# Kernel optimization log

Measured on AMD Instinct MI355X. Metric: run time of the kernel, lower is better.

The kernel has to match this reference:

```python
import jax, jax.numpy as jnp
import numpy as np

D1, D2, HIDDEN, BATCH = 8, 8, 256, 131072
SCALE_LIMIT = 1.0


def _mlp(h, w1, b1, w2, b2, w3, b3):
    # Linear-ReLU-Linear-ReLU-Linear, torch Linear convention: y = h @ W.T + b
    h = jax.nn.relu(h @ w1.T + b1)
    h = jax.nn.relu(h @ w2.T + b2)
    return h @ w3.T + b3


def setup_inputs() -> dict:
    key = jax.random.key(0)
    ks = jax.random.split(key, 25)
    inp = {"x": jax.random.normal(ks[0], (BATCH, D1 + D2), dtype=jnp.float32)}
    i = 1
    for net, d_in, d_out in (("s1", D2, D1), ("t1", D2, D1), ("s2", D1, D2), ("t2", D1, D2)):
        for lname, (o, nin) in (("1", (HIDDEN, d_in)), ("2", (HIDDEN, HIDDEN)), ("3", (d_out, HIDDEN))):
            lim = 1.0 / np.sqrt(nin)  # torch default init range
            inp[f"{net}_w{lname}"] = jax.random.uniform(ks[i], (o, nin), jnp.float32, -lim, lim); i += 1
            inp[f"{net}_b{lname}"] = jnp.zeros((o,), jnp.float32)
    return inp


def reference(x,
              s1_w1, s1_b1, s1_w2, s1_b2, s1_w3, s1_b3,
              t1_w1, t1_b1, t1_w2, t1_b2, t1_w3, t1_b3,
              s2_w1, s2_b1, s2_w2, s2_b2, s2_w3, s2_b3,
              t2_w1, t2_b1, t2_w2, t2_b2, t2_w3, t2_b3):
    x1, x2 = x[:, :D1], x[:, D1:]
    # first half-coupling: transform x1 conditioned on x2
    s2 = jnp.tanh(_mlp(x2, s1_w1, s1_b1, s1_w2, s1_b2, s1_w3, s1_b3)) * SCALE_LIMIT
    t2 = _mlp(x2, t1_w1, t1_b1, t1_w2, t1_b2, t1_w3, t1_b3)
    y1 = x1 * jnp.exp(s2) + t2
    # second half-coupling: transform x2 conditioned on y1
    s1 = jnp.tanh(_mlp(y1, s2_w1, s2_b1, s2_w2, s2_b2, s2_w3, s2_b3)) * SCALE_LIMIT
    t1 = _mlp(y1, t2_w1, t2_b1, t2_w2, t2_b2, t2_w3, t2_b3)
    y2 = x2 * jnp.exp(s1) + t1
    y = jnp.concatenate([y1, y2], axis=1)
    log_det = s2.sum(axis=1) + s1.sum(axis=1)
    return y, log_det
```

## Files before the change

### kernel.cpp

```cpp
#include <hip/hip_runtime.h>

#define BATCHN 131072
#define M_TILE 128
#define NTHREADS 1024
#define HPITCH 280
#define W2P_OFF 4096
#define W3P_OFF 73728
#define NET_STRIDE 77824
#define PACK_TOTAL (4 * NET_STRIDE)

typedef _Float16 hv8 __attribute__((ext_vector_type(8)));
typedef _Float16 hv4 __attribute__((ext_vector_type(4)));
typedef __fp16  fp16x2 __attribute__((ext_vector_type(2)));
typedef float f32x16 __attribute__((ext_vector_type(16)));
typedef float f32x4  __attribute__((ext_vector_type(4)));

struct __align__(16) SMEM {
    _Float16 xin[M_TILE][16];
    _Float16 Ha[M_TILE][HPITCH];
    _Float16 Hb[M_TILE][HPITCH];
    float s_tile[M_TILE][8];
    float t_tile[M_TILE][8];
    float ldet[M_TILE];
};

__global__ __launch_bounds__(256) void pack_weights(
    const float* __restrict__ s1w1, const float* __restrict__ s1b1, const float* __restrict__ s1w2, const float* __restrict__ s1b2, const float* __restrict__ s1w3,
    const float* __restrict__ t1w1, const float* __restrict__ t1b1, const float* __restrict__ t1w2, const float* __restrict__ t1b2, const float* __restrict__ t1w3,
    const float* __restrict__ s2w1, const float* __restrict__ s2b1, const float* __restrict__ s2w2, const float* __restrict__ s2b2, const float* __restrict__ s2w3,
    const float* __restrict__ t2w1, const float* __restrict__ t2b1, const float* __restrict__ t2w2, const float* __restrict__ t2b2, const float* __restrict__ t2w3,
    _Float16* __restrict__ wp)
{
    int tid = blockIdx.x * 256 + threadIdx.x;
    if (tid >= PACK_TOTAL) return;
    int net = tid / NET_STRIDE;
    int rem = tid - net * NET_STRIDE;
    const float* w1 = (net == 0) ? s1w1 : (net == 1) ? t1w1 : (net == 2) ? s2w1 : t2w1;
    const float* b1 = (net == 0) ? s1b1 : (net == 1) ? t1b1 : (net == 2) ? s2b1 : t2b1;
    const float* w2 = (net == 0) ? s1w2 : (net == 1) ? t1w2 : (net == 2) ? s2w2 : t2w2;
    const float* b2 = (net == 0) ? s1b2 : (net == 1) ? t1b2 : (net == 2) ? s2b2 : t2b2;
    const float* w3 = (net == 0) ? s1w3 : (net == 1) ? t1w3 : (net == 2) ? s2w3 : t2w3;
    float val;
    if (rem < W2P_OFF) {
        int nt = rem >> 9;
        int l  = (rem >> 3) & 63, j = rem & 7;
        int n  = nt * 32 + (l & 31);
        int k  = ((l >> 5) << 3) + j;
        val = (k < 8) ? w1[n * 8 + k] : (k == 8 ? b1[n] : 0.0f);
    } else if (rem < W3P_OFF) {
        int r = rem - W2P_OFF;
        int chunk = r >> 9;
        int nt = chunk / 17, ks = chunk - nt * 17;
        int l = (r >> 3) & 63, j = r & 7;
        int n = nt * 32 + (l & 31);
        int kk = ((l >> 5) << 3) + j;
        val = (ks < 16) ? w2[n * 256 + ks * 16 + kk] : (kk == 0 ? b2[n] : 0.0f);
    } else {
        int r = rem - W3P_OFF;
        int ks = r >> 9;
        int l = (r >> 3) & 63, j = r & 7;
        int n = l & 15;
        int k = ks * 32 + ((l >> 4) & 3) * 8 + j;
        val = (n < 8) ? w3[n * 256 + k] : 0.0f;
    }
    wp[tid] = (_Float16)val;
}

#define MFMA32(A,B,C) __builtin_amdgcn_mfma_f32_32x32x16_f16((A),(B),(C),0,0,0)

__device__ __forceinline__ void epi4(_Float16* __restrict__ dst, const f32x16& acc)
{
    #pragma unroll
    for (int q = 0; q < 4; ++q) {
        union { hv4 h4; fp16x2 h2[2]; } u;
        u.h2[0] = __builtin_amdgcn_cvt_pkrtz(fmaxf(acc[4*q+0], 0.f), fmaxf(acc[4*q+1], 0.f));
        u.h2[1] = __builtin_amdgcn_cvt_pkrtz(fmaxf(acc[4*q+2], 0.f), fmaxf(acc[4*q+3], 0.f));
        *(hv4*)(dst + 8 * q) = u.h4;
    }
}

__device__ __forceinline__ void layer1(const _Float16* __restrict__ wp, SMEM& sm,
                                       int nt, int mt, int lane, int l31, int hi)
{
    hv8 a  = *(const hv8*)(wp + nt * 512 + lane * 8);
    hv8 b0 = *(const hv8*)(&sm.xin[mt * 64 + l31][hi * 8]);
    hv8 b1 = *(const hv8*)(&sm.xin[mt * 64 + 32 + l31][hi * 8]);
    f32x16 z = {};
    f32x16 acc0 = MFMA32(a, b0, z);
    f32x16 acc1 = MFMA32(a, b1, z);
    epi4(&sm.Ha[mt * 64 + l31][nt * 32 + 4 * hi], acc0);
    epi4(&sm.Ha[mt * 64 + 32 + l31][nt * 32 + 4 * hi], acc1);
}

__device__ __forceinline__ void layer2(const _Float16* __restrict__ wp, SMEM& sm,
                                       int nt, int mt, int lane, int l31, int hi)
{
    const _Float16* __restrict__ w2 = wp + W2P_OFF + nt * (17 * 512);
    hv8 w[17];
    #pragma unroll
    for (int ks = 0; ks < 17; ++ks) w[ks] = *(const hv8*)(w2 + ks * 512 + lane * 8);
    const _Float16* __restrict__ bb0 = &sm.Ha[mt * 64 + l31][hi * 8];
    const _Float16* __restrict__ bb1 = &sm.Ha[mt * 64 + 32 + l31][hi * 8];
    f32x16 acc0 = {}, acc1 = {};
    #pragma unroll
    for (int ks = 0; ks < 17; ++ks) {
        hv8 b0 = *(const hv8*)(bb0 + ks * 16);
        hv8 b1 = *(const hv8*)(bb1 + ks * 16);
        acc0 = MFMA32(w[ks], b0, acc0);
        acc1 = MFMA32(w[ks], b1, acc1);
    }
    epi4(&sm.Hb[mt * 64 + l31][nt * 32 + 4 * hi], acc0);
    epi4(&sm.Hb[mt * 64 + 32 + l31][nt * 32 + 4 * hi], acc1);
}

template <bool IS_S>
__device__ __forceinline__ void layer3(const _Float16* __restrict__ wp, const float* __restrict__ b3,
                                       SMEM& sm, float (*__restrict__ stile)[8],
                                       int wave, int lane)
{
    if (wave >= 8) return;
    const _Float16* __restrict__ w3 = wp + W3P_OFF;
    const int l15 = lane & 15, q = lane >> 4;
    const int m = wave * 16 + l15;
    hv8 w[8];
    #pragma unroll
    for (int ks = 0; ks < 8; ++ks) w[ks] = *(const hv8*)(w3 + ks * 512 + lane * 8);
    const _Float16* __restrict__ bb = &sm.Hb[m][q * 8];
    f32x4 acc = {};
    #pragma unroll
    for (int ks = 0; ks < 8; ++ks)
        acc = __builtin_amdgcn_mfma_f32_16x16x32_f16(w[ks], *(const hv8*)(bb + ks * 32), acc, 0, 0, 0);
    if (q < 2) {
        float4 bv = *(const float4*)(b3 + q * 4);
        float o0 = acc[0] + bv.x, o1 = acc[1] + bv.y, o2 = acc[2] + bv.z, o3 = acc[3] + bv.w;
        if (IS_S) { o0 = tanhf(o0); o1 = tanhf(o1); o2 = tanhf(o2); o3 = tanhf(o3); }
        *(float4*)&stile[m][q * 4] = make_float4(o0, o1, o2, o3);
    }
}

__device__ __forceinline__ void stage(const _Float16* __restrict__ wpS, const float* __restrict__ b3S,
                                      const _Float16* __restrict__ wpT, const float* __restrict__ b3T,
                                      SMEM& sm,
                                      int wave, int nt, int mt, int lane, int l31, int hi)
{
    layer1(wpS, sm, nt, mt, lane, l31, hi);
    __syncthreads();
    layer2(wpS, sm, nt, mt, lane, l31, hi);
    __syncthreads();
    layer1(wpT, sm, nt, mt, lane, l31, hi);
    layer3<true >(wpS, b3S, sm, sm.s_tile, wave, lane);
    __syncthreads();
    layer2(wpT, sm, nt, mt, lane, l31, hi);
    __syncthreads();
    layer3<false>(wpT, b3T, sm, sm.t_tile, wave, lane);
    __syncthreads();
}

__global__ __launch_bounds__(NTHREADS, 4) void coupling_kernel(
    const float* __restrict__ x, const _Float16* __restrict__ wp,
    const float* __restrict__ s1b3, const float* __restrict__ t1b3,
    const float* __restrict__ s2b3, const float* __restrict__ t2b3,
    float* __restrict__ out)
{
    __shared__ SMEM sm;
    const int tid  = threadIdx.x;
    const int wave = tid >> 6, lane = tid & 63;
    const int l31  = lane & 31, hi = lane >> 5;
    const int mt   = wave & 1, nt = wave >> 1;
    const long row0 = (long)blockIdx.x * M_TILE;

    #pragma unroll
    for (int e = tid; e < M_TILE * 16; e += NTHREADS) {
        int row = e >> 4, c = e & 15;
        float v = (c < 8) ? x[(row0 + row) * 16 + 8 + c] : (c == 8 ? 1.0f : 0.0f);
        sm.xin[row][c] = (_Float16)v;
        sm.Ha[row][256 + c] = (c == 0) ? (_Float16)1.0f : (_Float16)0.0f;
    }
    __syncthreads();

    stage(wp + 0 * NET_STRIDE, s1b3, wp + 1 * NET_STRIDE, t1b3, sm, wave, nt, mt, lane, l31, hi);

    {
        int row = tid >> 3, c = tid & 7;
        float s = sm.s_tile[row][c];
        float t = sm.t_tile[row][c];
        float x1 = x[(row0 + row) * 16 + c];
        float y = x1 * expf(s) + t;
        out[(row0 + row) * 16 + c] = y;
        sm.xin[row][c] = (_Float16)y;
    }
    if (tid < M_TILE) {
        float a = 0.f;
        #pragma unroll
        for (int c = 0; c < 8; ++c) a += sm.s_tile[tid][c];
        sm.ldet[tid] = a;
    }
    __syncthreads();

    stage(wp + 2 * NET_STRIDE, s2b3, wp + 3 * NET_STRIDE, t2b3, sm, wave, nt, mt, lane, l31, hi);

    {
        int row = tid >> 3, c = tid & 7;
        float s = sm.s_tile[row][c];
        float t = sm.t_tile[row][c];
        float x2 = x[(row0 + row) * 16 + 8 + c];
        out[(row0 + row) * 16 + 8 + c] = x2 * expf(s) + t;
    }
    if (tid < M_TILE) {
        float a = sm.ldet[tid];
        #pragma unroll
        for (int c = 0; c < 8; ++c) a += sm.s_tile[tid][c];
        out[(long)BATCHN * 16 + row0 + tid] = a;
    }
}

extern "C" void kernel_launch(void* const* d_in, const int* in_sizes, int n_in,
                              void* d_out, int out_size, void* d_ws, size_t ws_size,
                              hipStream_t stream)
{
    const float* x = (const float*)d_in[0];
    const float* s1w1 = (const float*)d_in[1];  const float* s1b1 = (const float*)d_in[2];
    const float* s1w2 = (const float*)d_in[3];  const float* s1b2 = (const float*)d_in[4];
    const float* s1w3 = (const float*)d_in[5];  const float* s1b3 = (const float*)d_in[6];
    const float* t1w1 = (const float*)d_in[7];  const float* t1b1 = (const float*)d_in[8];
    const float* t1w2 = (const float*)d_in[9];  const float* t1b2 = (const float*)d_in[10];
    const float* t1w3 = (const float*)d_in[11]; const float* t1b3 = (const float*)d_in[12];
    const float* s2w1 = (const float*)d_in[13]; const float* s2b1 = (const float*)d_in[14];
    const float* s2w2 = (const float*)d_in[15]; const float* s2b2 = (const float*)d_in[16];
    const float* s2w3 = (const float*)d_in[17]; const float* s2b3 = (const float*)d_in[18];
    const float* t2w1 = (const float*)d_in[19]; const float* t2b1 = (const float*)d_in[20];
    const float* t2w2 = (const float*)d_in[21]; const float* t2b2 = (const float*)d_in[22];
    const float* t2w3 = (const float*)d_in[23]; const float* t2b3 = (const float*)d_in[24];

    _Float16* wp = (_Float16*)d_ws;

    pack_weights<<<(PACK_TOTAL + 255) / 256, 256, 0, stream>>>(
        s1w1, s1b1, s1w2, s1b2, s1w3,
        t1w1, t1b1, t1w2, t1b2, t1w3,
        s2w1, s2b1, s2w2, s2b2, s2w3,
        t2w1, t2b1, t2w2, t2b2, t2w3, wp);

    coupling_kernel<<<BATCHN / M_TILE, NTHREADS, 0, stream>>>(
        x, wp, s1b3, t1b3, s2b3, t2b3, (float*)d_out);
}
```

Baseline: 196.1 us.

## Halve block to 512 threads with 2x2 MFMA register tiles per wave

Block size drops from 1024 to 512 threads, so each wave now computes a 64x64 output tile (two N-tiles by two M-tiles) instead of 64x32. The goal is to reuse each LDS B-operand load across two weight fragments, and the W2 pack layout is reordered to interleave pairs of N-tiles. W2 weights (34 fragments) are preloaded into registers before layer1 so the global loads overlap with layer1 and the barrier. This raises register pressure, with launch bounds lowered to 2 blocks per CU and 34 hv8 live registers, which may reduce occupancy.

```diff
diff --git a/kernel.cpp b/kernel.cpp
--- a/kernel.cpp
+++ b/kernel.cpp
@@ -2,7 +2,7 @@
 
 #define BATCHN 131072
 #define M_TILE 128
-#define NTHREADS 1024
+#define NTHREADS 512
 #define HPITCH 280
 #define W2P_OFF 4096
 #define W3P_OFF 73728
@@ -50,7 +50,9 @@
     } else if (rem < W3P_OFF) {
         int r = rem - W2P_OFF;
         int chunk = r >> 9;
-        int nt = chunk / 17, ks = chunk - nt * 17;
+        int g = chunk / 34, rr = chunk - g * 34;
+        int ks = rr >> 1, s = rr & 1;
+        int nt = 2 * g + s;
         int l = (r >> 3) & 63, j = r & 7;
         int n = nt * 32 + (l & 31);
         int kk = ((l >> 5) << 3) + j;
@@ -79,38 +81,59 @@
     }
 }
 
+__device__ __forceinline__ void preloadW2(const _Float16* __restrict__ w2pp, int lane, hv8 (&w)[34])
+{
+    #pragma unroll
+    for (int i = 0; i < 34; ++i) w[i] = *(const hv8*)(w2pp + i * 512 + lane * 8);
+}
+
 __device__ __forceinline__ void layer1(const _Float16* __restrict__ wp, SMEM& sm,
-                                       int nt, int mt, int lane, int l31, int hi)
-{
-    hv8 a  = *(const hv8*)(wp + nt * 512 + lane * 8);
-    hv8 b0 = *(const hv8*)(&sm.xin[mt * 64 + l31][hi * 8]);
-    hv8 b1 = *(const hv8*)(&sm.xin[mt * 64 + 32 + l31][hi * 8]);
+                                       int g, int h, int lane, int l31, int hi)
+{
+    hv8 a0 = *(const hv8*)(wp + (2 * g + 0) * 512 + lane * 8);
+    hv8 a1 = *(const hv8*)(wp + (2 * g + 1) * 512 + lane * 8);
+    const int m0 = h * 64 + l31, m1 = m0 + 32;
+    hv8 b0 = *(const hv8*)(&sm.xin[m0][hi * 8]);
+    hv8 b1 = *(const hv8*)(&sm.xin[m1][hi * 8]);
     f32x16 z = {};
-    f32x16 acc0 = MFMA32(a, b0, z);
-    f32x16 acc1 = MFMA32(a, b1, z);
-    epi4(&sm.Ha[mt * 64 + l31][nt * 32 + 4 * hi], acc0);
-    epi4(&sm.Ha[mt * 64 + 32 + l31][nt * 32 + 4 * hi], acc1);
-}
-
-__device__ __forceinline__ void layer2(const _Float16* __restrict__ wp, SMEM& sm,
-                                       int nt, int mt, int lane, int l31, int hi)
-{
-    const _Float16* __restrict__ w2 = wp + W2P_OFF + nt * (17 * 512);
-    hv8 w[17];
-    #pragma unroll
-    for (int ks = 0; ks < 17; ++ks) w[ks] = *(const hv8*)(w2 + ks * 512 + lane * 8);
-    const _Float16* __restrict__ bb0 = &sm.Ha[mt * 64 + l31][hi * 8];
-    const _Float16* __restrict__ bb1 = &sm.Ha[mt * 64 + 32 + l31][hi * 8];
-    f32x16 acc0 = {}, acc1 = {};
-    #pragma unroll
-    for (int ks = 0; ks < 17; ++ks) {
+    f32x16 a00 = MFMA32(a0, b0, z);
+    f32x16 a10 = MFMA32(a1, b0, z);
+    f32x16 a01 = MFMA32(a0, b1, z);
+    f32x16 a11 = MFMA32(a1, b1, z);
+    epi4(&sm.Ha[m0][g * 64 +      4 * hi], a00);
+    epi4(&sm.Ha[m0][g * 64 + 32 + 4 * hi], a10);
+    epi4(&sm.Ha[m1][g * 64 +      4 * hi], a01);
+    epi4(&sm.Ha[m1][g * 64 + 32 + 4 * hi], a11);
+}
+
+__device__ __forceinline__ void layer2(const hv8 (&w)[34], SMEM& sm,
+                                       int g, int h, int l31, int hi)
+{
+    const int m0 = h * 64 + l31, m1 = m0 + 32;
+    const _Float16* __restrict__ bb0 = &sm.Ha[m0][hi * 8];
+    const _Float16* __restrict__ bb1 = &sm.Ha[m1][hi * 8];
+    f32x16 a00 = {}, a10 = {}, a01 = {}, a11 = {};
+    #pragma unroll
+    for (int ks = 0; ks < 16; ++ks) {
         hv8 b0 = *(const hv8*)(bb0 + ks * 16);
         hv8 b1 = *(const hv8*)(bb1 + ks * 16);
-        acc0 = MFMA32(w[ks], b0, acc0);
-        acc1 = MFMA32(w[ks], b1, acc1);
-    }
-    epi4(&sm.Hb[mt * 64 + l31][nt * 32 + 4 * hi], acc0);
-    epi4(&sm.Hb[mt * 64 + 32 + l31][nt * 32 + 4 * hi], acc1);
+        a00 = MFMA32(w[2*ks+0], b0, a00);
+        a10 = MFMA32(w[2*ks+1], b0, a10);
+        a01 = MFMA32(w[2*ks+0], b1, a01);
+        a11 = MFMA32(w[2*ks+1], b1, a11);
+    }
+    {
+        hv8 b0 = *(const hv8*)(&sm.Ha[m0][256 + hi * 8]);
+        hv8 b1 = *(const hv8*)(&sm.Ha[m1][256 + hi * 8]);
+        a00 = MFMA32(w[32], b0, a00);
+        a10 = MFMA32(w[33], b0, a10);
+        a01 = MFMA32(w[32], b1, a01);
+        a11 = MFMA32(w[33], b1, a11);
+    }
+    epi4(&sm.Hb[m0][g * 64 +      4 * hi], a00);
+    epi4(&sm.Hb[m0][g * 64 + 32 + 4 * hi], a10);
+    epi4(&sm.Hb[m1][g * 64 +      4 * hi], a01);
+    epi4(&sm.Hb[m1][g * 64 + 32 + 4 * hi], a11);
 }
 
 template <bool IS_S>
@@ -118,18 +141,16 @@
                                        SMEM& sm, float (*__restrict__ stile)[8],
                                        int wave, int lane)
 {
-    if (wave >= 8) return;
     const _Float16* __restrict__ w3 = wp + W3P_OFF;
     const int l15 = lane & 15, q = lane >> 4;
     const int m = wave * 16 + l15;
-    hv8 w[8];
-    #pragma unroll
-    for (int ks = 0; ks < 8; ++ks) w[ks] = *(const hv8*)(w3 + ks * 512 + lane * 8);
     const _Float16* __restrict__ bb = &sm.Hb[m][q * 8];
     f32x4 acc = {};
     #pragma unroll
-    for (int ks = 0; ks < 8; ++ks)
-        acc = __builtin_amdgcn_mfma_f32_16x16x32_f16(w[ks], *(const hv8*)(bb + ks * 32), acc, 0, 0, 0);
+    for (int ks = 0; ks < 8; ++ks) {
+        hv8 a = *(const hv8*)(w3 + ks * 512 + lane * 8);
+        acc = __builtin_amdgcn_mfma_f32_16x16x32_f16(a, *(const hv8*)(bb + ks * 32), acc, 0, 0, 0);
+    }
     if (q < 2) {
         float4 bv = *(const float4*)(b3 + q * 4);
         float o0 = acc[0] + bv.x, o1 = acc[1] + bv.y, o2 = acc[2] + bv.z, o3 = acc[3] + bv.w;
@@ -141,22 +162,30 @@
 __device__ __forceinline__ void stage(const _Float16* __restrict__ wpS, const float* __restrict__ b3S,
                                       const _Float16* __restrict__ wpT, const float* __restrict__ b3T,
                                       SMEM& sm,
-                                      int wave, int nt, int mt, int lane, int l31, int hi)
-{
-    layer1(wpS, sm, nt, mt, lane, l31, hi);
-    __syncthreads();
-    layer2(wpS, sm, nt, mt, lane, l31, hi);
-    __syncthreads();
-    layer1(wpT, sm, nt, mt, lane, l31, hi);
-    layer3<true >(wpS, b3S, sm, sm.s_tile, wave, lane);
-    __syncthreads();
-    layer2(wpT, sm, nt, mt, lane, l31, hi);
-    __syncthreads();
+                                      int wave, int g, int h, int lane, int l31, int hi)
+{
+    {
+        hv8 w[34];
+        preloadW2(wpS + W2P_OFF + g * (34 * 512), lane, w);
+        layer1(wpS, sm, g, h, lane, l31, hi);
+        __syncthreads();
+        layer2(w, sm, g, h, l31, hi);
+        __syncthreads();
+    }
+    {
+        hv8 w[34];
+        preloadW2(wpT + W2P_OFF + g * (34 * 512), lane, w);
+        layer1(wpT, sm, g, h, lane, l31, hi);
+        layer3<true >(wpS, b3S, sm, sm.s_tile, wave, lane);
+        __syncthreads();
+        layer2(w, sm, g, h, l31, hi);
+        __syncthreads();
+    }
     layer3<false>(wpT, b3T, sm, sm.t_tile, wave, lane);
     __syncthreads();
 }
 
-__global__ __launch_bounds__(NTHREADS, 4) void coupling_kernel(
+__global__ __launch_bounds__(NTHREADS, 2) void coupling_kernel(
     const float* __restrict__ x, const _Float16* __restrict__ wp,
     const float* __restrict__ s1b3, const float* __restrict__ t1b3,
     const float* __restrict__ s2b3, const float* __restrict__ t2b3,
@@ -166,7 +195,7 @@
     const int tid  = threadIdx.x;
     const int wave = tid >> 6, lane = tid & 63;
     const int l31  = lane & 31, hi = lane >> 5;
-    const int mt   = wave & 1, nt = wave >> 1;
+    const int g    = wave & 3, h = wave >> 2;
     const long row0 = (long)blockIdx.x * M_TILE;
 
     #pragma unroll
@@ -178,10 +207,11 @@
     }
     __syncthreads();
 
-    stage(wp + 0 * NET_STRIDE, s1b3, wp + 1 * NET_STRIDE, t1b3, sm, wave, nt, mt, lane, l31, hi);
-
-    {
-        int row = tid >> 3, c = tid & 7;
+    stage(wp + 0 * NET_STRIDE, s1b3, wp + 1 * NET_STRIDE, t1b3, sm, wave, g, h, lane, l31, hi);
+
+    #pragma unroll
+    for (int e = tid; e < M_TILE * 8; e += NTHREADS) {
+        int row = e >> 3, c = e & 7;
         float s = sm.s_tile[row][c];
         float t = sm.t_tile[row][c];
         float x1 = x[(row0 + row) * 16 + c];
@@ -197,10 +227,11 @@
     }
     __syncthreads();
 
-    stage(wp + 2 * NET_STRIDE, s2b3, wp + 3 * NET_STRIDE, t2b3, sm, wave, nt, mt, lane, l31, hi);
-
-    {
-        int row = tid >> 3, c = tid & 7;
+    stage(wp + 2 * NET_STRIDE, s2b3, wp + 3 * NET_STRIDE, t2b3, sm, wave, g, h, lane, l31, hi);
+
+    #pragma unroll
+    for (int e = tid; e < M_TILE * 8; e += NTHREADS) {
+        int row = e >> 3, c = e & 7;
         float s = sm.s_tile[row][c];
         float t = sm.t_tile[row][c];
         float x2 = x[(row0 + row) * 16 + 8 + c];
```

New measurement: 204.8 us. 4.5% more time.
